# Optimization experiments

Hardware: AMD Instinct MI355X
Metric: run time of the kernel (lower is better)

## Reference

```python
import jax, jax.numpy as jnp
import numpy as np

N_HEAD = 12

def fillnan(x):
    return jnp.nan_to_num(x, nan=0.0, posinf=0.0, neginf=0.0)

def setup_inputs() -> dict:
    key = jax.random.key(0)
    k1, k2, k3 = jax.random.split(key, 3)
    B, T, C = 2, 2048, 768
    x = jax.random.normal(k1, (B, T, C), dtype=jnp.float32)
    W_attn = jax.random.normal(k2, (3 * C, C), dtype=jnp.float32) * 0.02
    W_proj = jax.random.normal(k3, (C, C), dtype=jnp.float32) * 0.02
    return {"x": x, "W_attn": W_attn, "W_proj": W_proj}

def reference(x, W_attn, W_proj):
    B, T, C = x.shape
    H = N_HEAD
    D = C // H
    # qkv projection (torch Linear: x @ W^T), then nan-sanitize
    qkv = fillnan(jnp.einsum('btc,fc->btf', x, W_attn))  # [B,T,3C]
    q, k, v = jnp.split(qkv, 3, axis=-1)
    # [B,T,C] -> [B,H,T,D]
    q = q.reshape(B, T, H, D).transpose(0, 2, 1, 3)
    k = k.reshape(B, T, H, D).transpose(0, 2, 1, 3)
    v = v.reshape(B, T, H, D).transpose(0, 2, 1, 3)
    scale = 1.0 / np.sqrt(D).astype(np.float32)
    att = jnp.einsum('bhqd,bhkd->bhqk', q, k) * scale  # [B,H,T,T]
    att = fillnan(att)
    causal = jnp.tril(jnp.ones((T, T), dtype=bool))
    att = jnp.where(causal[None, None], att, -jnp.inf)
    att = jax.nn.softmax(att, axis=-1)
    att = fillnan(att)
    y = jnp.einsum('bhqk,bhkd->bhqd', att, v)  # [B,H,T,D]
    y = fillnan(y)
    y = y.transpose(0, 2, 1, 3).reshape(B, T, C)
    y = fillnan(jnp.einsum('btc,fc->btf', y, W_proj))
    return y
```

## Files before the change

### kernel.cpp

```cpp
#include <hip/hip_runtime.h>

typedef __attribute__((ext_vector_type(8))) short bf16x8;
typedef __attribute__((ext_vector_type(4))) float f32x4;

__device__ __forceinline__ unsigned short f2b(float f) {
  union { float f; unsigned u; } v; v.f = f;
  return (unsigned short)((v.u + 0x7FFFu + ((v.u >> 16) & 1u)) >> 16);
}

#define XN4   786432
#define WAN4  442368
#define WPN4  147456
__global__ void cvt_all(const float* __restrict__ x, const float* __restrict__ Wa,
                        const float* __restrict__ Wp,
                        unsigned short* __restrict__ xb, unsigned short* __restrict__ Wab,
                        unsigned short* __restrict__ Wpb) {
  int i = blockIdx.x * 256 + threadIdx.x;
  const float* src; unsigned short* dst; int off;
  if (i < XN4)            { src = x;  dst = xb;  off = i; }
  else if (i < XN4 + WAN4){ src = Wa; dst = Wab; off = i - XN4; }
  else                    { src = Wp; dst = Wpb; off = i - XN4 - WAN4; }
  float4 f = reinterpret_cast<const float4*>(src)[off];
  ushort4 o;
  o.x = f2b(f.x); o.y = f2b(f.y); o.z = f2b(f.z); o.w = f2b(f.w);
  reinterpret_cast<ushort4*>(dst)[off] = o;
}

#define BM 128
#define BN 128
#define BK 64

__global__ __launch_bounds__(256, 2)
void gemm_nt(const unsigned short* __restrict__ A,
             const unsigned short* __restrict__ Bm,
             int M, int N, int K, int mode,
             unsigned short* __restrict__ qb,
             unsigned short* __restrict__ kb_,
             unsigned short* __restrict__ vt,
             float* __restrict__ outf) {
  __shared__ unsigned short As[BM * BK];
  __shared__ unsigned short Bs[BN * BK];
  int tid = threadIdx.x;
  int wave = tid >> 6, lane = tid & 63;
  int quad = lane >> 4, l16 = lane & 15;
  int m0 = blockIdx.x * BM, n0 = blockIdx.y * BN;
  int wm = (wave & 1) * 64, wn = (wave >> 1) * 64;

  int srow = lane >> 3;
  int scol = ((lane & 7) ^ srow) << 3;

  f32x4 acc[4][4] = {};

  for (int k0 = 0; k0 < K; k0 += BK) {
    __syncthreads();
#pragma unroll
    for (int i = 0; i < 4; ++i) {
      int r = wave * 32 + i * 8;
      __builtin_amdgcn_global_load_lds(
          (const __attribute__((address_space(1))) unsigned int*)(A + (size_t)(m0 + r + srow) * K + k0 + scol),
          (__attribute__((address_space(3))) unsigned int*)(As + r * BK), 16, 0, 0);
      __builtin_amdgcn_global_load_lds(
          (const __attribute__((address_space(1))) unsigned int*)(Bm + (size_t)(n0 + r + srow) * K + k0 + scol),
          (__attribute__((address_space(3))) unsigned int*)(Bs + r * BK), 16, 0, 0);
    }
    __syncthreads();
#pragma unroll
    for (int kb = 0; kb < 2; ++kb) {
      int ch = (((kb << 2) | quad) ^ (l16 & 7)) << 3;
      bf16x8 af[4], bf[4];
#pragma unroll
      for (int i = 0; i < 4; ++i)
        af[i] = *reinterpret_cast<const bf16x8*>(As + (wm + i * 16 + l16) * BK + ch);
#pragma unroll
      for (int j = 0; j < 4; ++j)
        bf[j] = *reinterpret_cast<const bf16x8*>(Bs + (wn + j * 16 + l16) * BK + ch);
#pragma unroll
      for (int i = 0; i < 4; ++i)
#pragma unroll
        for (int j = 0; j < 4; ++j)
          acc[i][j] = __builtin_amdgcn_mfma_f32_16x16x32_bf16(af[i], bf[j], acc[i][j], 0, 0, 0);
    }
  }

  const float scale2 = 0.125f * 1.44269504089f;
#pragma unroll
  for (int i = 0; i < 4; ++i) {
    int mbase = m0 + wm + i * 16 + quad * 4;
#pragma unroll
    for (int j = 0; j < 4; ++j) {
      int f = n0 + wn + j * 16 + l16;
#pragma unroll
      for (int r = 0; r < 4; ++r) {
        float c = acc[i][j][r];
        int m = mbase + r;
        if (mode == 0) {
          int b = m >> 11, t = m & 2047;
          int which = f / 768;
          int f2 = f - which * 768;
          int h = f2 >> 6, d = f2 & 63;
          int bh = b * 12 + h;
          if (which == 0)      qb[((size_t)(bh * 2048 + t)) * 64 + d] = f2b(c * scale2);
          else if (which == 1) kb_[((size_t)(bh * 2048 + t)) * 64 + d] = f2b(c);
          else                 vt[((size_t)(bh * 64 + d)) * 2048 + t] = f2b(c);
        } else {
          outf[(size_t)m * N + f] = c;
        }
      }
    }
  }
}

__global__ __launch_bounds__(256, 4)
void attn_part(const unsigned short* __restrict__ Qb,
               const unsigned short* __restrict__ Kb,
               const unsigned short* __restrict__ Vt,
               float* __restrict__ Opart, float* __restrict__ Lpart) {
  __shared__ unsigned short Ks[2][64 * 64];
  __shared__ unsigned short Vs[2][64 * 64];
  const int T = 2048, D = 64;
  int lane = threadIdx.x & 63;
  int wave = threadIdx.x >> 6;
  int quad = lane >> 4, l16 = lane & 15;

  int w = blockIdx.x;
  int bh = w / 40;
  int r = 39 - (w - bh * 40);
  int qb, ci;
  if (r < 4)       { qb = r;                 ci = 0; }
  else if (r < 12) { qb = 4 + ((r - 4) >> 1);  ci = (r - 4) & 1; }
  else if (r < 24) { qb = 8 + (r - 12) / 3;    ci = (r - 12) % 3; }
  else             { qb = 12 + ((r - 24) >> 2); ci = (r - 24) & 3; }
  int nk = 2 * qb + 2;
  int nc = (qb >> 2) + 1;
  int t0 = ci * nk / nc, t1 = (ci + 1) * nk / nc;

  int q0 = qb * 128;
  int qrow = q0 + wave * 32;

  const unsigned short* Qp = Qb + (size_t)bh * T * D;
  const unsigned short* Kp = Kb + (size_t)bh * T * D;
  const unsigned short* Vp = Vt + (size_t)bh * D * T;

  int srow = lane >> 3;
  int scol = ((lane & 7) ^ srow) << 3;

  bf16x8 aq[2][2];
#pragma unroll
  for (int qi = 0; qi < 2; ++qi)
#pragma unroll
    for (int cc = 0; cc < 2; ++cc)
      aq[qi][cc] = *reinterpret_cast<const bf16x8*>(
          Qp + (qrow + qi * 16 + l16) * D + cc * 32 + quad * 8);

  bf16x8 ones;
#pragma unroll
  for (int e = 0; e < 8; ++e) ones[e] = (short)0x3F80;

  f32x4 o[2][4] = {};
  f32x4 lacc[2] = {};

  int hi = (lane >> 5) & 1;
  int adr0 = (((lane >> 4) & 1) * 32 + l16) << 2;
  int adr1 = adr0 + (16 << 2);

#define STAGE_KV(buf, k0s)                                                          \
  {                                                                                 \
    _Pragma("unroll")                                                               \
    for (int i_ = 0; i_ < 2; ++i_) {                                                \
      int rr_ = wave * 16 + i_ * 8;                                                 \
      __builtin_amdgcn_global_load_lds(                                             \
          (const __attribute__((address_space(1))) unsigned int*)(Kp + (size_t)((k0s) + rr_ + srow) * 64 + scol), \
          (__attribute__((address_space(3))) unsigned int*)(&Ks[buf][rr_ * 64]), 16, 0, 0); \
      __builtin_amdgcn_global_load_lds(                                             \
          (const __attribute__((address_space(1))) unsigned int*)(Vp + (size_t)(rr_ + srow) * 2048 + (k0s) + scol), \
          (__attribute__((address_space(3))) unsigned int*)(&Vs[buf][rr_ * 64]), 16, 0, 0); \
    }                                                                               \
  }

  STAGE_KV(0, t0 << 6);
  asm volatile("s_waitcnt vmcnt(0)" ::: "memory");
  __builtin_amdgcn_s_barrier();

  int cur = 0;
  for (int t = t0; t < t1; ++t) {
    int k0 = t << 6;
    if (t + 1 < t1) STAGE_KV(cur ^ 1, (t + 1) << 6);

    if (k0 <= qrow + 31) {
      f32x4 st[4][2] = {};
      __builtin_amdgcn_s_setprio(1);
#pragma unroll
      for (int kt = 0; kt < 4; ++kt) {
        bf16x8 ak0 = *reinterpret_cast<const bf16x8*>(Ks[cur] + (kt * 16 + l16) * 64 + ((quad ^ (l16 & 7)) << 3));
        bf16x8 ak1 = *reinterpret_cast<const bf16x8*>(Ks[cur] + (kt * 16 + l16) * 64 + (((4 | quad) ^ (l16 & 7)) << 3));
#pragma unroll
        for (int qi = 0; qi < 2; ++qi) {
          st[kt][qi] = __builtin_amdgcn_mfma_f32_16x16x32_bf16(ak0, aq[qi][0], st[kt][qi], 0, 0, 0);
          st[kt][qi] = __builtin_amdgcn_mfma_f32_16x16x32_bf16(ak1, aq[qi][1], st[kt][qi], 0, 0, 0);
        }
      }
      __builtin_amdgcn_s_setprio(0);

      if (k0 + 63 > qrow) {
#pragma unroll
        for (int kt = 0; kt < 4; ++kt)
#pragma unroll
          for (int qi = 0; qi < 2; ++qi) {
            int q = qrow + qi * 16 + l16;
#pragma unroll
            for (int rr = 0; rr < 4; ++rr) {
              int key = k0 + kt * 16 + quad * 4 + rr;
              st[kt][qi][rr] = (key <= q) ? st[kt][qi][rr] : -1e30f;
            }
          }
      }
#pragma unroll
      for (int kt = 0; kt < 4; ++kt)
#pragma unroll
        for (int qi = 0; qi < 2; ++qi)
#pragma unroll
          for (int rr = 0; rr < 4; ++rr)
            st[kt][qi][rr] = __builtin_amdgcn_exp2f(st[kt][qi][rr]);

      bf16x8 vf[4][2];
#pragma unroll
      for (int dt = 0; dt < 4; ++dt) {
        vf[dt][0] = *reinterpret_cast<const bf16x8*>(Vs[cur] + (dt * 16 + l16) * 64 + ((quad ^ (l16 & 7)) << 3));
        vf[dt][1] = *reinterpret_cast<const bf16x8*>(Vs[cur] + (dt * 16 + l16) * 64 + (((4 | quad) ^ (l16 & 7)) << 3));
      }

      bf16x8 pa[2][2];
#pragma unroll
      for (int qi = 0; qi < 2; ++qi) {
        int pk[4][2];
#pragma unroll
        for (int kt = 0; kt < 4; ++kt)
#pragma unroll
          for (int h = 0; h < 2; ++h)
            asm("v_cvt_pk_bf16_f32 %0, %1, %2"
                : "=v"(pk[kt][h])
                : "v"(st[kt][qi][2 * h]), "v"(st[kt][qi][2 * h + 1]));
#pragma unroll
        for (int g = 0; g < 2; ++g) {
          int wv[4];
#pragma unroll
          for (int w1 = 0; w1 < 2; ++w1)
#pragma unroll
            for (int w0 = 0; w0 < 2; ++w0) {
              int a_ = w1 ? adr1 : adr0;
              int r0_ = __builtin_amdgcn_ds_bpermute(a_, pk[2 * g + 0][w0]);
              int r1_ = __builtin_amdgcn_ds_bpermute(a_, pk[2 * g + 1][w0]);
              wv[w1 * 2 + w0] = hi ? r1_ : r0_;
            }
          union { int i[4]; bf16x8 v; } u_;
          u_.i[0] = wv[0]; u_.i[1] = wv[1]; u_.i[2] = wv[2]; u_.i[3] = wv[3];
          pa[qi][g] = u_.v;
        }
      }

      __builtin_amdgcn_s_setprio(1);
#pragma unroll
      for (int qi = 0; qi < 2; ++qi) {
#pragma unroll
        for (int dt = 0; dt < 4; ++dt) {
          o[qi][dt] = __builtin_amdgcn_mfma_f32_16x16x32_bf16(pa[qi][0], vf[dt][0], o[qi][dt], 0, 0, 0);
          o[qi][dt] = __builtin_amdgcn_mfma_f32_16x16x32_bf16(pa[qi][1], vf[dt][1], o[qi][dt], 0, 0, 0);
        }
        lacc[qi] = __builtin_amdgcn_mfma_f32_16x16x32_bf16(pa[qi][0], ones, lacc[qi], 0, 0, 0);
        lacc[qi] = __builtin_amdgcn_mfma_f32_16x16x32_bf16(pa[qi][1], ones, lacc[qi], 0, 0, 0);
      }
      __builtin_amdgcn_s_setprio(0);
    }

    asm volatile("s_waitcnt vmcnt(0)" ::: "memory");
    __builtin_amdgcn_s_barrier();
    cur ^= 1;
  }

  float* Op = Opart + (size_t)blockIdx.x * 8192 + wave * 32 * 64;
#pragma unroll
  for (int qi = 0; qi < 2; ++qi)
#pragma unroll
    for (int dt = 0; dt < 4; ++dt)
#pragma unroll
      for (int rr = 0; rr < 4; ++rr)
        Op[(qi * 16 + quad * 4 + rr) * 64 + dt * 16 + l16] = o[qi][dt][rr];
  if (l16 == 0) {
#pragma unroll
    for (int qi = 0; qi < 2; ++qi)
#pragma unroll
      for (int rr = 0; rr < 4; ++rr)
        Lpart[blockIdx.x * 128 + wave * 32 + qi * 16 + quad * 4 + rr] = lacc[qi][rr];
  }
}

__global__ __launch_bounds__(256)
void attn_combine(const float* __restrict__ Opart, const float* __restrict__ Lpart,
                  unsigned short* __restrict__ Yb) {
  int blk = blockIdx.x;
  int bh = blk >> 4, qb = blk & 15;
  int off = (qb < 4) ? qb : (qb < 8) ? 4 + 2 * (qb - 4)
          : (qb < 12) ? 12 + 3 * (qb - 8) : 24 + 4 * (qb - 12);
  int nc = (qb >> 2) + 1;
  int b = bh / 12, h = bh - b * 12;
  int q0 = qb * 128;
#pragma unroll
  for (int i = 0; i < 8; ++i) {
    int idx = i * 256 + threadIdx.x;
    int row = idx >> 4, c4 = idx & 15;
    float4 s = {0.f, 0.f, 0.f, 0.f};
    float L = 0.f;
    for (int ci = 0; ci < nc; ++ci) {
      size_t pb = (size_t)(bh * 40 + 39 - (off + ci));
      float4 v = *reinterpret_cast<const float4*>(Opart + pb * 8192 + row * 64 + c4 * 4);
      s.x += v.x; s.y += v.y; s.z += v.z; s.w += v.w;
      L += Lpart[pb * 128 + row];
    }
    float rl = 1.0f / L;
    ushort4 y;
    y.x = f2b(s.x * rl); y.y = f2b(s.y * rl);
    y.z = f2b(s.z * rl); y.w = f2b(s.w * rl);
    *reinterpret_cast<ushort4*>(Yb + ((size_t)(b * 2048 + q0 + row)) * 768 + h * 64 + c4 * 4) = y;
  }
}

extern "C" void kernel_launch(void* const* d_in, const int* in_sizes, int n_in,
                              void* d_out, int out_size, void* d_ws, size_t ws_size,
                              hipStream_t stream) {
  const float* x  = (const float*)d_in[0];
  const float* Wa = (const float*)d_in[1];
  const float* Wp = (const float*)d_in[2];
  float* out = (float*)d_out;

  unsigned short* ws = (unsigned short*)d_ws;
  unsigned short* xb  = ws;
  unsigned short* Wab = xb  + 3145728;
  unsigned short* Wpb = Wab + 1769472;
  unsigned short* Qb  = Wpb + 589824;
  unsigned short* Kb  = Qb  + 3145728;
  unsigned short* Vt  = Kb  + 3145728;
  unsigned short* Yb  = Vt  + 3145728;
  float*          Opart = (float*)(Yb + 3145728);
  float*          Lpart = Opart + 7864320;

  cvt_all<<<(XN4 + WAN4 + WPN4) / 256, 256, 0, stream>>>(x, Wa, Wp, xb, Wab, Wpb);

  gemm_nt<<<dim3(4096 / BM, 2304 / BN), 256, 0, stream>>>(
      xb, Wab, 4096, 2304, 768, 0, Qb, Kb, Vt, nullptr);

  attn_part<<<960, 256, 0, stream>>>(Qb, Kb, Vt, Opart, Lpart);
  attn_combine<<<384, 256, 0, stream>>>(Opart, Lpart, Yb);

  gemm_nt<<<dim3(4096 / BM, 768 / BN), 256, 0, stream>>>(
      Yb, Wpb, 4096, 768, 768, 1, nullptr, nullptr, nullptr, out);
}
```

Measured before the change: 169.1 us.

## Drop LDS K/V staging in attention; load fragments directly from global

The attention partial kernel no longer stages K and V tiles into double-buffered shared memory with barriers. Each wave now loads its MFMA K and V operand fragments straight from global memory, relying on L2/cache reuse across waves. Each wave also clips its loop at its own causal limit instead of skipping masked tiles inside the loop. Block indices are remapped with an XCD-style swizzle (blockIdx&7), and the occupancy hint drops from 4 to 3. The barriers and LDS traffic go away, at the cost of redundant global loads per wave and the exposed latency of register loads.

```diff
diff --git a/kernel.cpp b/kernel.cpp
--- a/kernel.cpp
+++ b/kernel.cpp
@@ -110,19 +110,17 @@
   }
 }
 
-__global__ __launch_bounds__(256, 4)
+__global__ __launch_bounds__(256, 3)
 void attn_part(const unsigned short* __restrict__ Qb,
                const unsigned short* __restrict__ Kb,
                const unsigned short* __restrict__ Vt,
                float* __restrict__ Opart, float* __restrict__ Lpart) {
-  __shared__ unsigned short Ks[2][64 * 64];
-  __shared__ unsigned short Vs[2][64 * 64];
   const int T = 2048, D = 64;
   int lane = threadIdx.x & 63;
   int wave = threadIdx.x >> 6;
   int quad = lane >> 4, l16 = lane & 15;
 
-  int w = blockIdx.x;
+  int w = (blockIdx.x & 7) * 120 + (blockIdx.x >> 3);
   int bh = w / 40;
   int r = 39 - (w - bh * 40);
   int qb, ci;
@@ -136,14 +134,13 @@
 
   int q0 = qb * 128;
   int qrow = q0 + wave * 32;
+  int tcl = ((qrow + 31) >> 6) + 1;
+  int tlim = t1 < tcl ? t1 : tcl;
 
   const unsigned short* Qp = Qb + (size_t)bh * T * D;
   const unsigned short* Kp = Kb + (size_t)bh * T * D;
   const unsigned short* Vp = Vt + (size_t)bh * D * T;
 
-  int srow = lane >> 3;
-  int scol = ((lane & 7) ^ srow) << 3;
-
   bf16x8 aq[2][2];
 #pragma unroll
   for (int qi = 0; qi < 2; ++qi)
@@ -163,121 +160,102 @@
   int adr0 = (((lane >> 4) & 1) * 32 + l16) << 2;
   int adr1 = adr0 + (16 << 2);
 
-#define STAGE_KV(buf, k0s)                                                          \
-  {                                                                                 \
-    _Pragma("unroll")                                                               \
-    for (int i_ = 0; i_ < 2; ++i_) {                                                \
-      int rr_ = wave * 16 + i_ * 8;                                                 \
-      __builtin_amdgcn_global_load_lds(                                             \
-          (const __attribute__((address_space(1))) unsigned int*)(Kp + (size_t)((k0s) + rr_ + srow) * 64 + scol), \
-          (__attribute__((address_space(3))) unsigned int*)(&Ks[buf][rr_ * 64]), 16, 0, 0); \
-      __builtin_amdgcn_global_load_lds(                                             \
-          (const __attribute__((address_space(1))) unsigned int*)(Vp + (size_t)(rr_ + srow) * 2048 + (k0s) + scol), \
-          (__attribute__((address_space(3))) unsigned int*)(&Vs[buf][rr_ * 64]), 16, 0, 0); \
-    }                                                                               \
-  }
-
-  STAGE_KV(0, t0 << 6);
-  asm volatile("s_waitcnt vmcnt(0)" ::: "memory");
-  __builtin_amdgcn_s_barrier();
-
-  int cur = 0;
-  for (int t = t0; t < t1; ++t) {
+  for (int t = t0; t < tlim; ++t) {
     int k0 = t << 6;
-    if (t + 1 < t1) STAGE_KV(cur ^ 1, (t + 1) << 6);
-
-    if (k0 <= qrow + 31) {
-      f32x4 st[4][2] = {};
-      __builtin_amdgcn_s_setprio(1);
-#pragma unroll
-      for (int kt = 0; kt < 4; ++kt) {
-        bf16x8 ak0 = *reinterpret_cast<const bf16x8*>(Ks[cur] + (kt * 16 + l16) * 64 + ((quad ^ (l16 & 7)) << 3));
-        bf16x8 ak1 = *reinterpret_cast<const bf16x8*>(Ks[cur] + (kt * 16 + l16) * 64 + (((4 | quad) ^ (l16 & 7)) << 3));
+    const unsigned short* Kt = Kp + (size_t)k0 * D;
+
+    bf16x8 ak[4][2];
+#pragma unroll
+    for (int kt = 0; kt < 4; ++kt)
+#pragma unroll
+      for (int cc = 0; cc < 2; ++cc)
+        ak[kt][cc] = *reinterpret_cast<const bf16x8*>(
+            Kt + (kt * 16 + l16) * D + cc * 32 + quad * 8);
+
+    f32x4 st[4][2] = {};
+    __builtin_amdgcn_s_setprio(1);
+#pragma unroll
+    for (int kt = 0; kt < 4; ++kt)
+#pragma unroll
+      for (int qi = 0; qi < 2; ++qi) {
+        st[kt][qi] = __builtin_amdgcn_mfma_f32_16x16x32_bf16(ak[kt][0], aq[qi][0], st[kt][qi], 0, 0, 0);
+        st[kt][qi] = __builtin_amdgcn_mfma_f32_16x16x32_bf16(ak[kt][1], aq[qi][1], st[kt][qi], 0, 0, 0);
+      }
+    __builtin_amdgcn_s_setprio(0);
+
+    bf16x8 vf[4][2];
+#pragma unroll
+    for (int dt = 0; dt < 4; ++dt)
+#pragma unroll
+      for (int g = 0; g < 2; ++g)
+        vf[dt][g] = *reinterpret_cast<const bf16x8*>(
+            Vp + (size_t)(dt * 16 + l16) * T + k0 + g * 32 + quad * 8);
+
+    if (k0 + 63 > qrow) {
+#pragma unroll
+      for (int kt = 0; kt < 4; ++kt)
 #pragma unroll
         for (int qi = 0; qi < 2; ++qi) {
-          st[kt][qi] = __builtin_amdgcn_mfma_f32_16x16x32_bf16(ak0, aq[qi][0], st[kt][qi], 0, 0, 0);
-          st[kt][qi] = __builtin_amdgcn_mfma_f32_16x16x32_bf16(ak1, aq[qi][1], st[kt][qi], 0, 0, 0);
+          int q = qrow + qi * 16 + l16;
+#pragma unroll
+          for (int rr = 0; rr < 4; ++rr) {
+            int key = k0 + kt * 16 + quad * 4 + rr;
+            st[kt][qi][rr] = (key <= q) ? st[kt][qi][rr] : -1e30f;
+          }
         }
+    }
+#pragma unroll
+    for (int kt = 0; kt < 4; ++kt)
+#pragma unroll
+      for (int qi = 0; qi < 2; ++qi)
+#pragma unroll
+        for (int rr = 0; rr < 4; ++rr)
+          st[kt][qi][rr] = __builtin_amdgcn_exp2f(st[kt][qi][rr]);
+
+    bf16x8 pa[2][2];
+#pragma unroll
+    for (int qi = 0; qi < 2; ++qi) {
+      int pk[4][2];
+#pragma unroll
+      for (int kt = 0; kt < 4; ++kt)
+#pragma unroll
+        for (int h = 0; h < 2; ++h)
+          asm("v_cvt_pk_bf16_f32 %0, %1, %2"
+              : "=v"(pk[kt][h])
+              : "v"(st[kt][qi][2 * h]), "v"(st[kt][qi][2 * h + 1]));
+#pragma unroll
+      for (int g = 0; g < 2; ++g) {
+        int wv[4];
+#pragma unroll
+        for (int w1 = 0; w1 < 2; ++w1)
+#pragma unroll
+          for (int w0 = 0; w0 < 2; ++w0) {
+            int a_ = w1 ? adr1 : adr0;
+            int r0_ = __builtin_amdgcn_ds_bpermute(a_, pk[2 * g + 0][w0]);
+            int r1_ = __builtin_amdgcn_ds_bpermute(a_, pk[2 * g + 1][w0]);
+            wv[w1 * 2 + w0] = hi ? r1_ : r0_;
+          }
+        union { int i[4]; bf16x8 v; } u_;
+        u_.i[0] = wv[0]; u_.i[1] = wv[1]; u_.i[2] = wv[2]; u_.i[3] = wv[3];
+        pa[qi][g] = u_.v;
       }
-      __builtin_amdgcn_s_setprio(0);
-
-      if (k0 + 63 > qrow) {
-#pragma unroll
-        for (int kt = 0; kt < 4; ++kt)
-#pragma unroll
-          for (int qi = 0; qi < 2; ++qi) {
-            int q = qrow + qi * 16 + l16;
-#pragma unroll
-            for (int rr = 0; rr < 4; ++rr) {
-              int key = k0 + kt * 16 + quad * 4 + rr;
-              st[kt][qi][rr] = (key <= q) ? st[kt][qi][rr] : -1e30f;
-            }
-          }
+    }
+
+    __builtin_amdgcn_s_setprio(1);
+#pragma unroll
+    for (int qi = 0; qi < 2; ++qi) {
+#pragma unroll
+      for (int dt = 0; dt < 4; ++dt) {
+        o[qi][dt] = __builtin_amdgcn_mfma_f32_16x16x32_bf16(pa[qi][0], vf[dt][0], o[qi][dt], 0, 0, 0);
+        o[qi][dt] = __builtin_amdgcn_mfma_f32_16x16x32_bf16(pa[qi][1], vf[dt][1], o[qi][dt], 0, 0, 0);
       }
-#pragma unroll
-      for (int kt = 0; kt < 4; ++kt)
-#pragma unroll
-        for (int qi = 0; qi < 2; ++qi)
-#pragma unroll
-          for (int rr = 0; rr < 4; ++rr)
-            st[kt][qi][rr] = __builtin_amdgcn_exp2f(st[kt][qi][rr]);
-
-      bf16x8 vf[4][2];
-#pragma unroll
-      for (int dt = 0; dt < 4; ++dt) {
-        vf[dt][0] = *reinterpret_cast<const bf16x8*>(Vs[cur] + (dt * 16 + l16) * 64 + ((quad ^ (l16 & 7)) << 3));
-        vf[dt][1] = *reinterpret_cast<const bf16x8*>(Vs[cur] + (dt * 16 + l16) * 64 + (((4 | quad) ^ (l16 & 7)) << 3));
-      }
-
-      bf16x8 pa[2][2];
-#pragma unroll
-      for (int qi = 0; qi < 2; ++qi) {
-        int pk[4][2];
-#pragma unroll
-        for (int kt = 0; kt < 4; ++kt)
-#pragma unroll
-          for (int h = 0; h < 2; ++h)
-            asm("v_cvt_pk_bf16_f32 %0, %1, %2"
-                : "=v"(pk[kt][h])
-                : "v"(st[kt][qi][2 * h]), "v"(st[kt][qi][2 * h + 1]));
-#pragma unroll
-        for (int g = 0; g < 2; ++g) {
-          int wv[4];
-#pragma unroll
-          for (int w1 = 0; w1 < 2; ++w1)
-#pragma unroll
-            for (int w0 = 0; w0 < 2; ++w0) {
-              int a_ = w1 ? adr1 : adr0;
-              int r0_ = __builtin_amdgcn_ds_bpermute(a_, pk[2 * g + 0][w0]);
-              int r1_ = __builtin_amdgcn_ds_bpermute(a_, pk[2 * g + 1][w0]);
-              wv[w1 * 2 + w0] = hi ? r1_ : r0_;
-            }
-          union { int i[4]; bf16x8 v; } u_;
-          u_.i[0] = wv[0]; u_.i[1] = wv[1]; u_.i[2] = wv[2]; u_.i[3] = wv[3];
-          pa[qi][g] = u_.v;
-        }
-      }
-
-      __builtin_amdgcn_s_setprio(1);
-#pragma unroll
-      for (int qi = 0; qi < 2; ++qi) {
-#pragma unroll
-        for (int dt = 0; dt < 4; ++dt) {
-          o[qi][dt] = __builtin_amdgcn_mfma_f32_16x16x32_bf16(pa[qi][0], vf[dt][0], o[qi][dt], 0, 0, 0);
-          o[qi][dt] = __builtin_amdgcn_mfma_f32_16x16x32_bf16(pa[qi][1], vf[dt][1], o[qi][dt], 0, 0, 0);
-        }
-        lacc[qi] = __builtin_amdgcn_mfma_f32_16x16x32_bf16(pa[qi][0], ones, lacc[qi], 0, 0, 0);
-        lacc[qi] = __builtin_amdgcn_mfma_f32_16x16x32_bf16(pa[qi][1], ones, lacc[qi], 0, 0, 0);
-      }
-      __builtin_amdgcn_s_setprio(0);
-    }
-
-    asm volatile("s_waitcnt vmcnt(0)" ::: "memory");
-    __builtin_amdgcn_s_barrier();
-    cur ^= 1;
-  }
-
-  float* Op = Opart + (size_t)blockIdx.x * 8192 + wave * 32 * 64;
+      lacc[qi] = __builtin_amdgcn_mfma_f32_16x16x32_bf16(pa[qi][0], ones, lacc[qi], 0, 0, 0);
+      lacc[qi] = __builtin_amdgcn_mfma_f32_16x16x32_bf16(pa[qi][1], ones, lacc[qi], 0, 0, 0);
+    }
+    __builtin_amdgcn_s_setprio(0);
+  }
+
+  float* Op = Opart + (size_t)w * 8192 + wave * 32 * 64;
 #pragma unroll
   for (int qi = 0; qi < 2; ++qi)
 #pragma unroll
@@ -290,7 +268,7 @@
     for (int qi = 0; qi < 2; ++qi)
 #pragma unroll
       for (int rr = 0; rr < 4; ++rr)
-        Lpart[blockIdx.x * 128 + wave * 32 + qi * 16 + quad * 4 + rr] = lacc[qi][rr];
+        Lpart[w * 128 + wave * 32 + qi * 16 + quad * 4 + rr] = lacc[qi][rr];
   }
 }
 
```

New measurement: 194.8 us. +15.2%, slower.
